# Optimization experiments

Measured on AMD Instinct MI355X. Metric: run time of the kernel, lower is better.

The kernel has to match this reference:

```python
import jax, jax.numpy as jnp
from jax import lax
import numpy as np

B, P, M1, M2, M3 = 128, 168, 2, 2, 2
M = M1 * M2 * M3
HIDC, HIDR, HIDS, CK, SKIP, HW = 50, 50, 5, 6, 24, 24
PT = (P - CK) // SKIP  # int((P-Ck)/skip) = 6
L = P - CK + 1         # 163


def gru(xs, w_ih, w_hh, b_ih, b_hh, hid):
    # xs: [T, N, in]; torch nn.GRU cell semantics, h0 = 0. Returns final h: [N, hid].
    def step(h, x):
        gi = x @ w_ih.T + b_ih
        gh = h @ w_hh.T + b_hh
        ir, iz, inn = jnp.split(gi, 3, axis=-1)
        hr, hz, hn = jnp.split(gh, 3, axis=-1)
        r = jax.nn.sigmoid(ir + hr)
        z = jax.nn.sigmoid(iz + hz)
        n = jnp.tanh(inn + r * hn)
        return (1.0 - z) * n + z * h, None
    h0 = jnp.zeros((xs.shape[1], hid), xs.dtype)
    h, _ = lax.scan(step, h0, xs)
    return h


def setup_inputs() -> dict:
    key = jax.random.key(0)
    ks = jax.random.split(key, 16)
    O = P * HIDC * CK  # 50400 conv output channels
    d = {
        'x': jax.random.normal(ks[0], (B, P, M1, M2, M3), jnp.float32),
        'conv_w': jax.random.normal(ks[1], (O, P, M1, M2, M3), jnp.float32) * 0.02,
        'conv_b': jax.random.normal(ks[2], (O,), jnp.float32) * 0.02,
        'g1_wih': jax.random.normal(ks[3], (3 * HIDR, HIDC), jnp.float32) * 0.1,
        'g1_whh': jax.random.normal(ks[4], (3 * HIDR, HIDR), jnp.float32) * 0.1,
        'g1_bih': jax.random.normal(ks[5], (3 * HIDR,), jnp.float32) * 0.1,
        'g1_bhh': jax.random.normal(ks[6], (3 * HIDR,), jnp.float32) * 0.1,
        'gs_wih': jax.random.normal(ks[7], (3 * HIDS, HIDC), jnp.float32) * 0.1,
        'gs_whh': jax.random.normal(ks[8], (3 * HIDS, HIDS), jnp.float32) * 0.1,
        'gs_bih': jax.random.normal(ks[9], (3 * HIDS,), jnp.float32) * 0.1,
        'gs_bhh': jax.random.normal(ks[10], (3 * HIDS,), jnp.float32) * 0.1,
        'l1_w': jax.random.normal(ks[11], (M, HIDR + SKIP * HIDS), jnp.float32) * 0.1,
        'l1_b': jax.random.normal(ks[12], (M,), jnp.float32) * 0.1,
        'hw_w': jax.random.normal(ks[13], (1, HW), jnp.float32) * 0.1,
        'hw_b': jax.random.normal(ks[14], (1,), jnp.float32) * 0.1,
    }
    return d


def reference(x, conv_w, conv_b, g1_wih, g1_whh, g1_bih, g1_bhh,
              gs_wih, gs_whh, gs_bih, gs_bhh, l1_w, l1_b, hw_w, hw_b):
    # Conv3d with kernel == full spatial extent is a dense matmul over (P*m1*m2*m3).
    xf = x.reshape(B, -1)                       # [B, P*M]
    wf = conv_w.reshape(conv_w.shape[0], -1)    # [O, P*M]
    c = jax.nn.relu(xf @ wf.T + conv_b)         # [B, O]
    c = c.reshape(B, HIDC, CK, P)
    # Diagonal strided sum (the torch triple loop): res1[b,c,t] = sum_k c[b,c,k,k+t]
    res1 = sum(c[:, :, k, k:k + L] for k in range(CK))  # [B, HIDC, L]
    # dropout: eval mode (identity)
    r = gru(jnp.transpose(res1, (2, 0, 1)), g1_wih, g1_whh, g1_bih, g1_bhh, HIDR)  # [B, HIDR]
    # skip GRU
    s = res1[:, :, -PT * SKIP:]                          # [B, HIDC, PT*SKIP]
    s = s.reshape(B, HIDC, PT, SKIP)
    s = jnp.transpose(s, (2, 0, 3, 1)).reshape(PT, B * SKIP, HIDC)
    hs = gru(s, gs_wih, gs_whh, gs_bih, gs_bhh, HIDS)    # [B*SKIP, HIDS]
    hs = hs.reshape(B, SKIP * HIDS)
    r = jnp.concatenate([r, hs], axis=1)                 # [B, HIDR + SKIP*HIDS]
    res = r @ l1_w.T + l1_b                              # [B, M]
    # highway (AR) component over the last HW timesteps
    z = x[:, -HW:].reshape(B, HW, M)                     # [B, HW, M]
    z = jnp.transpose(z, (0, 2, 1)).reshape(-1, HW)      # [B*M, HW]
    z = z @ hw_w.T + hw_b                                # [B*M, 1]
    res = res + z.reshape(B, M)
    res = jax.nn.sigmoid(res)
    return res.reshape(B, M1, M2, M3)
```

## Files before the change

### kernel.cpp

```cpp
#include <hip/hip_runtime.h>
#include <hip/hip_bf16.h>
#include <cstdint>


typedef __attribute__((ext_vector_type(8))) short short8;
typedef __attribute__((ext_vector_type(4))) float f32x4;
typedef __attribute__((ext_vector_type(2))) float f32x2;

__device__ __forceinline__ unsigned short bf16rn(float f) {
    unsigned u = __float_as_uint(f);
    return (unsigned short)((u + 0x7FFFu + ((u >> 16) & 1u)) >> 16);
}
__device__ __forceinline__ unsigned pk2(float a, float b) {
    return ((unsigned)bf16rn(b) << 16) | (unsigned)bf16rn(a);
}
__device__ __forceinline__ uint4 pack8(float4 f0, float4 f1) {
    uint4 u;
    u.x = pk2(f0.x, f0.y); u.y = pk2(f0.z, f0.w);
    u.z = pk2(f1.x, f1.y); u.w = pk2(f1.z, f1.w);
    return u;
}
__device__ __forceinline__ float bf2f(unsigned short u) {
    return __uint_as_float((unsigned)u << 16);
}
__device__ __forceinline__ float sigmf(float x) {
    return __builtin_amdgcn_rcpf(1.f + __expf(-x));
}
__device__ __forceinline__ float tanhf_(float x) {
    return 1.f - 2.f * __builtin_amdgcn_rcpf(__expf(2.f * x) + 1.f);
}

__global__ __launch_bounds__(256, 2)
void k1_conv_gemm(const float* __restrict__ x, const float* __restrict__ w,
                  const float* __restrict__ bias, unsigned short* __restrict__ c) {
    __shared__ uint4 a_lds[8 * 129];
    __shared__ uint4 b_lds[8 * 113];
    const int tid  = threadIdx.x;
    const int n0   = blockIdx.x * 112;
    const int wave = tid >> 6, lane = tid & 63;
    const int quad = lane >> 4, m16 = lane & 15;

    f32x4 acc[2][7];
#pragma unroll
    for (int i = 0; i < 2; ++i)
#pragma unroll
        for (int j = 0; j < 7; ++j) acc[i][j] = (f32x4){0.f, 0.f, 0.f, 0.f};

    float4 pa[4][2];
    float4 pb[4][2];

    auto issue = [&](int kb) {
#pragma unroll
        for (int i = 0; i < 4; ++i) {
            int row = (tid >> 3) + 32 * i;
            const float* gp = x + row * 1344 + kb + (tid & 7) * 8;
            pa[i][0] = *reinterpret_cast<const float4*>(gp);
            pa[i][1] = *reinterpret_cast<const float4*>(gp + 4);
        }
#pragma unroll
        for (int i = 0; i < 4; ++i) {
            int idx = tid + 256 * i;
            if (idx < 896) {
                int row = idx >> 3;
                const float* gp = w + (size_t)(n0 + row) * 1344 + kb + (idx & 7) * 8;
                pb[i][0] = *reinterpret_cast<const float4*>(gp);
                pb[i][1] = *reinterpret_cast<const float4*>(gp + 4);
            }
        }
    };

    issue(0);
    for (int kb = 0; kb < 1344; kb += 64) {
#pragma unroll
        for (int i = 0; i < 4; ++i) {
            int idx = tid + 256 * i;
            int row = idx >> 3, ks = idx & 7;
            a_lds[ks * 129 + row] = pack8(pa[i][0], pa[i][1]);
        }
#pragma unroll
        for (int i = 0; i < 4; ++i) {
            int idx = tid + 256 * i;
            if (idx < 896) {
                int row = idx >> 3, ks = idx & 7;
                b_lds[ks * 113 + row] = pack8(pb[i][0], pb[i][1]);
            }
        }
        __syncthreads();
        if (kb + 64 < 1344) issue(kb + 64);
#pragma unroll
        for (int half = 0; half < 2; ++half) {
            const int kp = half * 4 + quad;
            short8 af[2], bfr[7];
#pragma unroll
            for (int rt = 0; rt < 2; ++rt)
                af[rt] = ((const short8*)a_lds)[kp * 129 + wave * 32 + rt * 16 + m16];
#pragma unroll
            for (int ct = 0; ct < 7; ++ct)
                bfr[ct] = ((const short8*)b_lds)[kp * 113 + ct * 16 + m16];
#pragma unroll
            for (int rt = 0; rt < 2; ++rt)
#pragma unroll
                for (int ct = 0; ct < 7; ++ct)
                    acc[rt][ct] = __builtin_amdgcn_mfma_f32_16x16x32_bf16(
                        af[rt], bfr[ct], acc[rt][ct], 0, 0, 0);
        }
        __syncthreads();
    }
#pragma unroll
    for (int ct = 0; ct < 7; ++ct) {
        int col = n0 + ct * 16 + m16;
        float bv = bias[col];
#pragma unroll
        for (int rt = 0; rt < 2; ++rt) {
#pragma unroll
            for (int r = 0; r < 4; ++r) {
                int grow = wave * 32 + rt * 16 + quad * 4 + r;
                float v = acc[rt][ct][r] + bv;
                v = fmaxf(v, 0.f);
                c[(size_t)grow * 50400 + col] = bf16rn(v);
            }
        }
    }
}

__global__ __launch_bounds__(384, 1)
void k_fused(const unsigned short* __restrict__ c,
             const float* __restrict__ g1_wih, const float* __restrict__ g1_whh,
             const float* __restrict__ g1_bih, const float* __restrict__ g1_bhh,
             const float* __restrict__ gs_wih, const float* __restrict__ gs_whh,
             const float* __restrict__ gs_bih, const float* __restrict__ gs_bhh,
             const float* __restrict__ l1_w, const float* __restrict__ l1_b,
             const float* __restrict__ x, const float* __restrict__ hw_w,
             const float* __restrict__ hw_b, float* __restrict__ out) {
    __shared__ float rloc[50 * 164];
    __shared__ float gi1l[163 * 150];
    __shared__ float gi2l[144 * 15];
    __shared__ float l1wl[8 * 170];
    __shared__ __align__(16) float hl[64];
    __shared__ float hsl[120];
    __shared__ float r1l[50];

    const int b    = blockIdx.x;
    const int tid  = threadIdx.x;
    const int wave = tid >> 6, lane = tid & 63;

    const unsigned short* cb = c + (size_t)b * 50400;
    for (int idx = tid; idx < 8150; idx += 384) {
        int hc = idx / 163, t = idx - hc * 163;
        int base = hc * 1008 + t;
        float s = 0.f;
#pragma unroll
        for (int k = 0; k < 6; ++k) s += bf2f(cb[base + 169 * k]);
        rloc[hc * 164 + t] = s;
    }
    for (int idx = tid; idx < 1360; idx += 384) l1wl[idx] = l1_w[idx];
    __syncthreads();

    {
        const int tB   = (wave >> 1) * 64 + lane;
        const int half = wave & 1;
        if (tB < 163) {
            float xcol[50];
#pragma unroll
            for (int j = 0; j < 50; ++j) xcol[j] = rloc[j * 164 + tB];

            const int c0 = __builtin_amdgcn_readfirstlane(half * 75);
            const float* wbase = g1_wih + c0 * 50;
            float* gdst = &gi1l[tB * 150 + c0];
            for (int cc = 0; cc < 75; ++cc) {
                const float* wp = wbase + cc * 50;
                float acc = g1_bih[c0 + cc];
#pragma unroll
                for (int j = 0; j < 50; ++j) acc += xcol[j] * wp[j];
                gdst[cc] = acc;
            }
            if (tB >= 19) {
                const int r2 = tB - 19;
                const int d0 = __builtin_amdgcn_readfirstlane(half * 8);
                const int ncol = half ? 7 : 8;
                float* g2 = &gi2l[r2 * 15];
                for (int cc = 0; cc < ncol; ++cc) {
                    const float* wp = gs_wih + (d0 + cc) * 50;
                    float acc = gs_bih[d0 + cc];
#pragma unroll
                    for (int j = 0; j < 50; ++j) acc += xcol[j] * wp[j];
                    g2[d0 + cc] = acc;
                }
            }
        }
    }
    __syncthreads();
    if (wave != 0) return;

    const int lc = (lane < 50) ? lane : 49;
    f32x2 wr2[25], wz2[25], wn2[25];
    {
        const float* wrp = g1_whh + lc * 50;
        const float* wzp = g1_whh + (50 + lc) * 50;
        const float* wnp = g1_whh + (100 + lc) * 50;
#pragma unroll
        for (int j = 0; j < 25; ++j) {
            wr2[j] = *reinterpret_cast<const f32x2*>(wrp + 2 * j);
            wz2[j] = *reinterpret_cast<const f32x2*>(wzp + 2 * j);
            wn2[j] = *reinterpret_cast<const f32x2*>(wnp + 2 * j);
        }
#pragma unroll
        for (int j = 0; j < 25; ++j) {
            asm volatile("" : "+v"(wr2[j]));
            asm volatile("" : "+v"(wz2[j]));
            asm volatile("" : "+v"(wn2[j]));
        }
    }
    const float bhr = g1_bhh[lc], bhz = g1_bhh[50 + lc], bhn = g1_bhh[100 + lc];
    hl[lane] = 0.f;
    float hcur = 0.f;
    const float* gp = gi1l;
    for (int t = 0; t < 163; ++t) {
        float gir = gp[lc], giz = gp[50 + lc], gin = gp[100 + lc];
        float4 h4[12];
#pragma unroll
        for (int j4 = 0; j4 < 12; ++j4)
            h4[j4] = *reinterpret_cast<const float4*>(&hl[4 * j4]);
        f32x2 ht; ht.x = hl[48]; ht.y = hl[49];
        f32x2 ar = {0.f, 0.f}, az = {0.f, 0.f}, an = {0.f, 0.f};
#pragma unroll
        for (int j4 = 0; j4 < 12; ++j4) {
            f32x2 h0; h0.x = h4[j4].x; h0.y = h4[j4].y;
            f32x2 h1; h1.x = h4[j4].z; h1.y = h4[j4].w;
            ar += wr2[2 * j4] * h0; ar += wr2[2 * j4 + 1] * h1;
            az += wz2[2 * j4] * h0; az += wz2[2 * j4 + 1] * h1;
            an += wn2[2 * j4] * h0; an += wn2[2 * j4 + 1] * h1;
        }
        ar += wr2[24] * ht; az += wz2[24] * ht; an += wn2[24] * ht;
        float rg = sigmf(gir + bhr + ar.x + ar.y);
        float zg = sigmf(giz + bhz + az.x + az.y);
        float ng = tanhf_(gin + rg * (bhn + an.x + an.y));
        hcur = (1.f - zg) * ng + zg * hcur;
        hl[lane] = hcur;
        gp += 150;
    }
    if (lane < 50) r1l[lane] = hcur;

    if (lane < 24) {
        float h2[5] = {0.f, 0.f, 0.f, 0.f, 0.f};
        for (int pt = 0; pt < 6; ++pt) {
            const float* g2 = &gi2l[(pt * 24 + lane) * 15];
            float gi[15];
#pragma unroll
            for (int i = 0; i < 15; ++i) gi[i] = g2[i];
            float gh[15];
#pragma unroll
            for (int i = 0; i < 15; ++i) {
                float s = gs_bhh[i];
#pragma unroll
                for (int j = 0; j < 5; ++j) s += gs_whh[i * 5 + j] * h2[j];
                gh[i] = s;
            }
#pragma unroll
            for (int u = 0; u < 5; ++u) {
                float rg = sigmf(gi[u] + gh[u]);
                float zg = sigmf(gi[5 + u] + gh[5 + u]);
                float ng = tanhf_(gi[10 + u] + rg * gh[10 + u]);
                h2[u] = (1.f - zg) * ng + zg * h2[u];
            }
        }
#pragma unroll
        for (int u = 0; u < 5; ++u) hsl[lane * 5 + u] = h2[u];
    }

    if (lane < 8) {
        const int m = lane;
        float acc = l1_b[m];
        const float* wrow = &l1wl[m * 170];
#pragma unroll
        for (int j = 0; j < 50; ++j) acc += r1l[j] * wrow[j];
#pragma unroll
        for (int j = 0; j < 120; ++j) acc += hsl[j] * wrow[50 + j];
        float z = hw_b[0];
        const float* xb = x + (size_t)b * 1344 + 144 * 8 + m;
#pragma unroll
        for (int wi = 0; wi < 24; ++wi) z += xb[wi * 8] * hw_w[wi];
        out[b * 8 + m] = __builtin_amdgcn_rcpf(1.f + __expf(-(acc + z)));
    }
}

extern "C" void kernel_launch(void* const* d_in, const int* in_sizes, int n_in,
                              void* d_out, int out_size, void* d_ws, size_t ws_size,
                              hipStream_t stream) {
    const float* x      = (const float*)d_in[0];
    const float* conv_w = (const float*)d_in[1];
    const float* conv_b = (const float*)d_in[2];
    const float* g1_wih = (const float*)d_in[3];
    const float* g1_whh = (const float*)d_in[4];
    const float* g1_bih = (const float*)d_in[5];
    const float* g1_bhh = (const float*)d_in[6];
    const float* gs_wih = (const float*)d_in[7];
    const float* gs_whh = (const float*)d_in[8];
    const float* gs_bih = (const float*)d_in[9];
    const float* gs_bhh = (const float*)d_in[10];
    const float* l1_w   = (const float*)d_in[11];
    const float* l1_b   = (const float*)d_in[12];
    const float* hw_w   = (const float*)d_in[13];
    const float* hw_b   = (const float*)d_in[14];
    float* out = (float*)d_out;

    unsigned short* c = (unsigned short*)d_ws;

    hipLaunchKernelGGL(k1_conv_gemm, dim3(450), dim3(256), 0, stream, x, conv_w, conv_b, c);
    hipLaunchKernelGGL(k_fused,      dim3(128), dim3(384), 0, stream,
                       c, g1_wih, g1_whh, g1_bih, g1_bhh,
                       gs_wih, gs_whh, gs_bih, gs_bhh,
                       l1_w, l1_b, x, hw_w, hw_b, out);
}
```

Before: 510.5 us.

## Split fused GRU kernel into projection and recurrence kernels via global workspace

Splits the fused per-batch kernel in two. The first kernel computes the GRU input projections and writes them to global workspace. The second, a single-wave kernel, runs the recurrent loop, reading the projections from global memory and prefetching the next timestep's values one step ahead. The aim is to stop the 384-thread block holding its large LDS allocation while only one wave runs the serial recurrence. The cost is an extra launch plus a global write and read of the projections, and the recurrence now depends on global-memory latency rather than LDS.

```diff
diff --git a/kernel.cpp b/kernel.cpp
--- a/kernel.cpp
+++ b/kernel.cpp
@@ -124,21 +124,13 @@
 }
 
 __global__ __launch_bounds__(384, 1)
-void k_fused(const unsigned short* __restrict__ c,
-             const float* __restrict__ g1_wih, const float* __restrict__ g1_whh,
-             const float* __restrict__ g1_bih, const float* __restrict__ g1_bhh,
-             const float* __restrict__ gs_wih, const float* __restrict__ gs_whh,
-             const float* __restrict__ gs_bih, const float* __restrict__ gs_bhh,
-             const float* __restrict__ l1_w, const float* __restrict__ l1_b,
-             const float* __restrict__ x, const float* __restrict__ hw_w,
-             const float* __restrict__ hw_b, float* __restrict__ out) {
+void k_proj(const unsigned short* __restrict__ c,
+            const float* __restrict__ g1_wih, const float* __restrict__ g1_bih,
+            const float* __restrict__ gs_wih, const float* __restrict__ gs_bih,
+            float* __restrict__ gi1g, float* __restrict__ gi2g) {
     __shared__ float rloc[50 * 164];
-    __shared__ float gi1l[163 * 150];
-    __shared__ float gi2l[144 * 15];
-    __shared__ float l1wl[8 * 170];
-    __shared__ __align__(16) float hl[64];
-    __shared__ float hsl[120];
-    __shared__ float r1l[50];
+    __shared__ __align__(8) float gi1l[163 * 150];
+    __shared__ __align__(8) float gi2l[144 * 15];
 
     const int b    = blockIdx.x;
     const int tid  = threadIdx.x;
@@ -153,7 +145,6 @@
         for (int k = 0; k < 6; ++k) s += bf2f(cb[base + 169 * k]);
         rloc[hc * 164 + t] = s;
     }
-    for (int idx = tid; idx < 1360; idx += 384) l1wl[idx] = l1_w[idx];
     __syncthreads();
 
     {
@@ -190,9 +181,33 @@
         }
     }
     __syncthreads();
-    if (wave != 0) return;
-
+
+    {
+        const float2* src = reinterpret_cast<const float2*>(gi1l);
+        float2* dst = reinterpret_cast<float2*>(gi1g + (size_t)b * 24450);
+        for (int i = tid; i < 12225; i += 384) dst[i] = src[i];
+        const float2* s2 = reinterpret_cast<const float2*>(gi2l);
+        float2* d2 = reinterpret_cast<float2*>(gi2g + (size_t)b * 2160);
+        for (int i = tid; i < 1080; i += 384) d2[i] = s2[i];
+    }
+}
+
+__global__ __launch_bounds__(64, 1)
+void k_gru(const float* __restrict__ gi1g, const float* __restrict__ g1_whh,
+           const float* __restrict__ g1_bhh,
+           const float* __restrict__ gi2g, const float* __restrict__ gs_whh,
+           const float* __restrict__ gs_bhh,
+           const float* __restrict__ l1_w, const float* __restrict__ l1_b,
+           const float* __restrict__ x, const float* __restrict__ hw_w,
+           const float* __restrict__ hw_b, float* __restrict__ out) {
+    __shared__ __align__(16) float hl[64];
+    __shared__ float r1l[50];
+    __shared__ float hsl[120];
+
+    const int b = blockIdx.x;
+    const int lane = threadIdx.x;
     const int lc = (lane < 50) ? lane : 49;
+
     f32x2 wr2[25], wz2[25], wn2[25];
     {
         const float* wrp = g1_whh + lc * 50;
@@ -214,9 +229,15 @@
     const float bhr = g1_bhh[lc], bhz = g1_bhh[50 + lc], bhn = g1_bhh[100 + lc];
     hl[lane] = 0.f;
     float hcur = 0.f;
-    const float* gp = gi1l;
+
+    const float* gp = gi1g + (size_t)b * 24450;
+    float gir = gp[lc], giz = gp[50 + lc], gin = gp[100 + lc];
     for (int t = 0; t < 163; ++t) {
-        float gir = gp[lc], giz = gp[50 + lc], gin = gp[100 + lc];
+        float ngir = 0.f, ngiz = 0.f, ngin = 0.f;
+        if (t < 162) {
+            const float* gq = gp + 150;
+            ngir = gq[lc]; ngiz = gq[50 + lc]; ngin = gq[100 + lc];
+        }
         float4 h4[12];
 #pragma unroll
         for (int j4 = 0; j4 < 12; ++j4)
@@ -237,14 +258,16 @@
         float ng = tanhf_(gin + rg * (bhn + an.x + an.y));
         hcur = (1.f - zg) * ng + zg * hcur;
         hl[lane] = hcur;
+        gir = ngir; giz = ngiz; gin = ngin;
         gp += 150;
     }
     if (lane < 50) r1l[lane] = hcur;
 
     if (lane < 24) {
         float h2[5] = {0.f, 0.f, 0.f, 0.f, 0.f};
+        const float* g2base = gi2g + (size_t)b * 2160;
         for (int pt = 0; pt < 6; ++pt) {
-            const float* g2 = &gi2l[(pt * 24 + lane) * 15];
+            const float* g2 = g2base + (pt * 24 + lane) * 15;
             float gi[15];
 #pragma unroll
             for (int i = 0; i < 15; ++i) gi[i] = g2[i];
@@ -271,7 +294,7 @@
     if (lane < 8) {
         const int m = lane;
         float acc = l1_b[m];
-        const float* wrow = &l1wl[m * 170];
+        const float* wrow = l1_w + m * 170;
 #pragma unroll
         for (int j = 0; j < 50; ++j) acc += r1l[j] * wrow[j];
 #pragma unroll
@@ -304,11 +327,15 @@
     const float* hw_b   = (const float*)d_in[14];
     float* out = (float*)d_out;
 
-    unsigned short* c = (unsigned short*)d_ws;
+    char* ws = (char*)d_ws;
+    unsigned short* c = (unsigned short*)ws;
+    float* gi1g       = (float*)(ws + 12902400);
+    float* gi2g       = (float*)(ws + 25420800);
 
     hipLaunchKernelGGL(k1_conv_gemm, dim3(450), dim3(256), 0, stream, x, conv_w, conv_b, c);
-    hipLaunchKernelGGL(k_fused,      dim3(128), dim3(384), 0, stream,
-                       c, g1_wih, g1_whh, g1_bih, g1_bhh,
-                       gs_wih, gs_whh, gs_bih, gs_bhh,
+    hipLaunchKernelGGL(k_proj,       dim3(128), dim3(384), 0, stream,
+                       c, g1_wih, g1_bih, gs_wih, gs_bih, gi1g, gi2g);
+    hipLaunchKernelGGL(k_gru,        dim3(128), dim3(64),  0, stream,
+                       gi1g, g1_whh, g1_bhh, gi2g, gs_whh, gs_bhh,
                        l1_w, l1_b, x, hw_w, hw_b, out);
 }
```

Result: no change. 516.7 us (+1.2%).
